# Performance work log

Measured on AMD Instinct MI355X. Metric: run time of the kernel, lower is better.

The kernel has to match this reference:

```python
import jax, jax.numpy as jnp
import numpy as np

B, C, H, W = 4, 64, 64, 64
CQK = C // 8


def setup_inputs() -> dict:
    key = jax.random.key(0)
    ks = jax.random.split(key, 4)
    x = jax.random.normal(ks[0], (B, C, H, W), dtype=jnp.float32)
    Wq = jax.random.normal(ks[1], (CQK, C), dtype=jnp.float32) * (1.0 / np.sqrt(C))
    bq = jnp.zeros((CQK,), dtype=jnp.float32)
    Wk = jax.random.normal(ks[2], (CQK, C), dtype=jnp.float32) * (1.0 / np.sqrt(C))
    bk = jnp.zeros((CQK,), dtype=jnp.float32)
    Wv = jax.random.normal(ks[3], (C, C), dtype=jnp.float32) * (1.0 / np.sqrt(C))
    bv = jnp.zeros((C,), dtype=jnp.float32)
    gamma = jnp.ones((1,), dtype=jnp.float32)
    return {"x": x, "Wq": Wq, "bq": bq, "Wk": Wk, "bk": bk,
            "Wv": Wv, "bv": bv, "gamma": gamma}


def reference(x, Wq, bq, Wk, bk, Wv, bv, gamma):
    b, c, h, w = x.shape
    n = h * w
    xf = x.reshape(b, c, n)                      # [B, C, N]
    # 1x1 convs == per-pixel linear over channels
    q = jnp.einsum('oc,bcn->bon', Wq, xf) + bq[:, None]   # [B, C/8, N]
    k = jnp.einsum('oc,bcn->bon', Wk, xf) + bk[:, None]   # [B, C/8, N]
    v = jnp.einsum('oc,bcn->bon', Wv, xf) + bv[:, None]   # [B, C, N]
    # attention_map[b,i,j] = <q[:, i], k[:, j]>; softmax over j
    attn = jax.nn.softmax(jnp.einsum('bci,bcj->bij', q, k), axis=-1)  # [B, N, N]
    # out[b,c,i] = sum_j v[b,c,j] * attn[b,i,j]  (bmm(V, attn^T))
    out = jnp.einsum('bcj,bij->bci', v, attn).reshape(b, c, h, w)
    return gamma * out + x
```

## Files before the change

kernel.cpp:

```cpp
#include <hip/hip_runtime.h>
#include <hip/hip_bf16.h>
#include <math.h>

#define NPIX 4096

typedef __attribute__((ext_vector_type(8))) short s8;
typedef __attribute__((ext_vector_type(16))) float f16v;

static __device__ __forceinline__ unsigned packbf2(float a, float b) {
    union { __hip_bfloat162 h; unsigned u; } x;
    x.h = __float22bfloat162_rn(make_float2(a, b));
    return x.u;
}
static __device__ __forceinline__ float fexp2(float x) {
#if __has_builtin(__builtin_amdgcn_exp2f)
    return __builtin_amdgcn_exp2f(x);
#else
    return exp2f(x);
#endif
}

static __device__ __forceinline__ void lane_swap(unsigned a, unsigned b, int lh,
                                                 unsigned &x, unsigned &y) {
#if __has_builtin(__builtin_amdgcn_permlane32_swap)
    auto r = __builtin_amdgcn_permlane32_swap((int)a, (int)b, false, false);
    x = (unsigned)r[0];
    y = (unsigned)r[1];
#else
    unsigned sa = __shfl_xor(a, 32), sb = __shfl_xor(b, 32);
    x = lh ? sb : a;
    y = lh ? b : sa;
#endif
}

__global__ __launch_bounds__(512) void prep_kernel(
    const float* __restrict__ x,
    const float* __restrict__ Wq, const float* __restrict__ bq,
    const float* __restrict__ Wk, const float* __restrict__ bk,
    __hip_bfloat16* __restrict__ qbf, __hip_bfloat16* __restrict__ kbf,
    __hip_bfloat16* __restrict__ xbf)
{
    __shared__ float Xp[64][65];
    __shared__ unsigned short Qs[64][8];
    int t = threadIdx.x;
    int p = t & 63;
    int g = t >> 6;
    int bid = blockIdx.x;
    int og = bid & 1;
    int n0 = ((bid >> 1) & 63) << 6;
    int b  = bid >> 7;

    const float* xb = x + ((size_t)b << 18);
    __hip_bfloat16* xbb = xbf + ((size_t)b << 18);
#pragma unroll
    for (int u = 0; u < 8; ++u) {
        int c = g + (u << 3);
        float v = xb[((size_t)c << 12) + n0 + p];
        Xp[c][p] = v;
        if ((og == 0) ? (u < 4) : (u >= 4))
            xbb[((size_t)c << 12) + n0 + p] = __float2bfloat16(v);
    }
    __syncthreads();

    const float* W  = og ? Wk : Wq;
    const float* bb = og ? bk : bq;
    const float* wr = W + g * 64;
    float acc = bb[g];
#pragma unroll
    for (int c = 0; c < 64; ++c) acc = fmaf(wr[c], Xp[c][p], acc);
    if (!og) acc *= 1.4426950408889634f;

    union { __hip_bfloat16 h; unsigned short u; } cv;
    cv.h = __float2bfloat16(acc);
    Qs[p][g] = cv.u;
    __syncthreads();

    if (t < 64) {
        __hip_bfloat16* dst = (og ? kbf : qbf) + ((size_t)(b * NPIX + n0 + t) << 3);
        *(s8*)dst = *(const s8*)&Qs[t][0];
    }
}

__global__ __launch_bounds__(512, 4) void flash_fused_kernel(
    const __hip_bfloat16* __restrict__ qbf, const __hip_bfloat16* __restrict__ kbf,
    const __hip_bfloat16* __restrict__ xbf,
    const float* __restrict__ Wv, const float* __restrict__ bv,
    const float* __restrict__ x, const float* __restrict__ gamma,
    float* __restrict__ out)
{
    __shared__ __align__(16) char pool[35200];
    unsigned short* Xs = (unsigned short*)pool;

    int t = threadIdx.x;
    int w    = t >> 6;
    int lane = t & 63;
    int l32  = lane & 31;
    int lh   = lane >> 5;

    int b  = blockIdx.x >> 7;
    int i0 = (blockIdx.x & 127) << 5;

    const s8 zero8 = {0, 0, 0, 0, 0, 0, 0, 0};

    s8 qf;
    {
        s8 qv = *(const s8*)(qbf + ((size_t)(b * NPIX + i0 + l32) << 3));
        qf = (lh == 0) ? qv : zero8;
    }

    f16v acc[2];
    f16v zero16;
#pragma unroll
    for (int r = 0; r < 16; ++r) { acc[0][r] = 0.f; acc[1][r] = 0.f; zero16[r] = 0.f; }
    float lsum = 0.f;

    const __hip_bfloat16* kb = kbf + ((size_t)(b * NPIX) << 3);
    const unsigned short* xg = (const unsigned short*)xbf + ((size_t)b << 18);

    int c = (w << 3) + (t & 7), seg = (t >> 3) & 7;
    const unsigned short* xsrc = xg + ((size_t)c << 12) + seg * 32;
    int xdst = c * 260 + seg * 32;

    uint2 pv[8];
    s8 kf;
    {
        const unsigned short* p = xsrc;
#pragma unroll
        for (int u = 0; u < 8; ++u) pv[u] = *(const uint2*)(p + u * 4);
        kf = *(const s8*)(kb + ((size_t)(w * 32 + l32) << 3));
    }

    for (int jt = 0; jt < 16; ++jt) {
        __syncthreads();

        {
            unsigned short* dstp = Xs + xdst;
#pragma unroll
            for (int u = 0; u < 8; ++u) *(uint2*)(dstp + u * 4) = pv[u];
        }

        f16v sC = __builtin_amdgcn_mfma_f32_32x32x16_bf16(kf, qf, zero16, 0, 0, 0);
        float e[16];
#pragma unroll
        for (int r = 0; r < 16; ++r) e[r] = fexp2(sC[r]);
#pragma unroll
        for (int r = 0; r < 16; ++r) lsum += e[r];
        unsigned P2[8];
#pragma unroll
        for (int s = 0; s < 8; ++s) P2[s] = packbf2(e[2 * s], e[2 * s + 1]);

        __syncthreads();

        {
            int jn = ((jt + 1) & 15) << 8;
            const unsigned short* p = xsrc + jn;
#pragma unroll
            for (int u = 0; u < 8; ++u) pv[u] = *(const uint2*)(p + u * 4);
            kf = *(const s8*)(kb + ((size_t)(jn + w * 32 + l32) << 3));
        }

        unsigned b00, b01, b02, b03, b10, b11, b12, b13;
        lane_swap(P2[0], P2[2], lh, b00, b02);
        lane_swap(P2[1], P2[3], lh, b01, b03);
        lane_swap(P2[4], P2[6], lh, b10, b12);
        lane_swap(P2[5], P2[7], lh, b11, b13);
        union { unsigned u[4]; s8 v; } bf0, bf1;
        bf0.u[0] = b00; bf0.u[1] = b01; bf0.u[2] = b02; bf0.u[3] = b03;
        bf1.u[0] = b10; bf1.u[1] = b11; bf1.u[2] = b12; bf1.u[3] = b13;

#pragma unroll
        for (int cm = 0; cm < 2; ++cm) {
            const unsigned short* xrow = Xs + (cm * 32 + l32) * 260 + w * 32 + lh * 8;
            union { uint2 u2[2]; s8 v; } xu0, xu1;
            xu0.u2[0] = *(const uint2*)(xrow);
            xu0.u2[1] = *(const uint2*)(xrow + 4);
            acc[cm] = __builtin_amdgcn_mfma_f32_32x32x16_bf16(xu0.v, bf0.v, acc[cm], 0, 0, 0);
            xu1.u2[0] = *(const uint2*)(xrow + 16);
            xu1.u2[1] = *(const uint2*)(xrow + 20);
            acc[cm] = __builtin_amdgcn_mfma_f32_32x32x16_bf16(xu1.v, bf1.v, acc[cm], 0, 0, 0);
        }
    }

    float* OshA = (float*)pool;
    float* OshB = (float*)(pool + 8704);
    float* Linv = (float*)(pool + 17408);
    float* bvs  = (float*)(pool + 17536);
    float* Wvs  = (float*)(pool + 17792);
    float* Lsh  = (float*)(pool + 34176);

    lsum += __shfl_xor(lsum, 32);
    if (lh == 0) Lsh[w * 32 + l32] = lsum;

    float* Og = (w >> 2) ? OshB : OshA;
    for (int s = 0; s < 4; ++s) {
        __syncthreads();
        if ((w & 3) == s) {
#pragma unroll
            for (int cm = 0; cm < 2; ++cm)
#pragma unroll
                for (int r = 0; r < 16; ++r) {
                    int cc = cm * 32 + (r & 3) + 8 * (r >> 2) + 4 * lh;
                    float* p = Og + l32 * 68 + cc;
                    if (s == 0) *p = acc[cm][r];
                    else        *p += acc[cm][r];
                }
        }
    }
    __syncthreads();

    if (t < 32) {
        float lt = 0.f;
#pragma unroll
        for (int ww = 0; ww < 8; ++ww) lt += Lsh[ww * 32 + t];
        Linv[t] = 1.0f / lt;
    }
    if (t < 64) bvs[t] = bv[t];
    {
        const float4* wsrc = (const float4*)Wv;
        float4* wdst = (float4*)Wvs;
        wdst[t] = wsrc[t];
        wdst[t + 512] = wsrc[t + 512];
    }
    __syncthreads();

    {
        int i  = t & 31;
        int cg = t >> 5;
        float inv = Linv[i];
        float res[4] = {0.f, 0.f, 0.f, 0.f};
#pragma unroll 4
        for (int cb = 0; cb < 16; ++cb) {
            float4 oa = *(const float4*)(OshA + i * 68 + cb * 4);
            float4 ob = *(const float4*)(OshB + i * 68 + cb * 4);
            float4 o = make_float4(oa.x + ob.x, oa.y + ob.y, oa.z + ob.z, oa.w + ob.w);
#pragma unroll
            for (int k = 0; k < 4; ++k) {
                const float4 wv4 = *(const float4*)(Wvs + (cg * 4 + k) * 64 + cb * 4);
                res[k] = fmaf(wv4.x, o.x, fmaf(wv4.y, o.y, fmaf(wv4.z, o.z, fmaf(wv4.w, o.w, res[k]))));
            }
        }
        float g = gamma[0];
        const float* xr = x + ((size_t)b << 18) + i0;
        float* outp = out + ((size_t)b << 18) + i0;
#pragma unroll
        for (int k = 0; k < 4; ++k) {
            int cch = cg * 4 + k;
            float attn = fmaf(res[k], inv, bvs[cch]);
            size_t off = ((size_t)cch << 12) + i;
            outp[off] = fmaf(g, attn, xr[off]);
        }
    }
}

extern "C" void kernel_launch(void* const* d_in, const int* in_sizes, int n_in,
                              void* d_out, int out_size, void* d_ws, size_t ws_size,
                              hipStream_t stream) {
    const float* x     = (const float*)d_in[0];
    const float* Wq    = (const float*)d_in[1];
    const float* bq    = (const float*)d_in[2];
    const float* Wk    = (const float*)d_in[3];
    const float* bk    = (const float*)d_in[4];
    const float* Wv    = (const float*)d_in[5];
    const float* bv    = (const float*)d_in[6];
    const float* gamma = (const float*)d_in[7];
    float* out = (float*)d_out;

    __hip_bfloat16* qbf = (__hip_bfloat16*)d_ws;
    __hip_bfloat16* kbf = qbf + (size_t)4 * NPIX * 8;
    __hip_bfloat16* xbf = kbf + (size_t)4 * NPIX * 8;

    prep_kernel<<<512, 512, 0, stream>>>(x, Wq, bq, Wk, bk, qbf, kbf, xbf);
    flash_fused_kernel<<<512, 512, 0, stream>>>(qbf, kbf, xbf, Wv, bv, x, gamma, out);
}
```

Measured before the change: 113.8 us.

## Double-buffer X tiles in LDS via direct global-to-LDS loads with XOR swizzle

Replaces the register-staged single LDS buffer for X tiles with two LDS buffers filled by global_load_lds, which copies straight from global memory into LDS. Padding is replaced by an XOR swizzle on the LDS layout, and each tile step now needs one barrier instead of two. Loads for tile jt+2 are issued while tile jt+1 is being consumed, which hides memory latency and saves VGPRs and LDS store instructions. The trade-off is that LDS use grows to 64 KB per block, which limits how many blocks can be resident on a CU. Correctness also depends on the barrier waiting for the asynchronous LDS loads to finish.

```diff
diff --git a/kernel.cpp b/kernel.cpp
--- a/kernel.cpp
+++ b/kernel.cpp
@@ -6,6 +6,9 @@
 
 typedef __attribute__((ext_vector_type(8))) short s8;
 typedef __attribute__((ext_vector_type(16))) float f16v;
+
+typedef __attribute__((address_space(1))) const void glob_cv;
+typedef __attribute__((address_space(3))) void lds_v;
 
 static __device__ __forceinline__ unsigned packbf2(float a, float b) {
     union { __hip_bfloat162 h; unsigned u; } x;
@@ -17,6 +20,15 @@
     return __builtin_amdgcn_exp2f(x);
 #else
     return exp2f(x);
+#endif
+}
+
+static __device__ __forceinline__ void gl_lds16(const unsigned short* g,
+                                                unsigned short* l, int lane) {
+#if __has_builtin(__builtin_amdgcn_global_load_lds)
+    __builtin_amdgcn_global_load_lds((glob_cv*)g, (lds_v*)l, 16, 0, 0);
+#else
+    *(uint4*)(l + lane * 8) = *(const uint4*)g;
 #endif
 }
 
@@ -88,8 +100,9 @@
     const float* __restrict__ x, const float* __restrict__ gamma,
     float* __restrict__ out)
 {
-    __shared__ __align__(16) char pool[35200];
-    unsigned short* Xs = (unsigned short*)pool;
+    __shared__ __align__(16) char pool[65536];
+    unsigned short* Xs0 = (unsigned short*)pool;
+    unsigned short* Xs1 = Xs0 + 16384;
 
     int t = threadIdx.x;
     int w    = t >> 6;
@@ -117,69 +130,72 @@
     const __hip_bfloat16* kb = kbf + ((size_t)(b * NPIX) << 3);
     const unsigned short* xg = (const unsigned short*)xbf + ((size_t)b << 18);
 
-    int c = (w << 3) + (t & 7), seg = (t >> 3) & 7;
-    const unsigned short* xsrc = xg + ((size_t)c << 12) + seg * 32;
-    int xdst = c * 260 + seg * 32;
-
-    uint2 pv[8];
-    s8 kf;
-    {
-        const unsigned short* p = xsrc;
-#pragma unroll
-        for (int u = 0; u < 8; ++u) pv[u] = *(const uint2*)(p + u * 4);
-        kf = *(const s8*)(kb + ((size_t)(w * 32 + l32) << 3));
-    }
-
-    for (int jt = 0; jt < 16; ++jt) {
-        __syncthreads();
-
-        {
-            unsigned short* dstp = Xs + xdst;
-#pragma unroll
-            for (int u = 0; u < 8; ++u) *(uint2*)(dstp + u * 4) = pv[u];
-        }
-
-        f16v sC = __builtin_amdgcn_mfma_f32_32x32x16_bf16(kf, qf, zero16, 0, 0, 0);
-        float e[16];
-#pragma unroll
-        for (int r = 0; r < 16; ++r) e[r] = fexp2(sC[r]);
-#pragma unroll
-        for (int r = 0; r < 16; ++r) lsum += e[r];
-        unsigned P2[8];
-#pragma unroll
-        for (int s = 0; s < 8; ++s) P2[s] = packbf2(e[2 * s], e[2 * s + 1]);
-
-        __syncthreads();
-
-        {
-            int jn = ((jt + 1) & 15) << 8;
-            const unsigned short* p = xsrc + jn;
-#pragma unroll
-            for (int u = 0; u < 8; ++u) pv[u] = *(const uint2*)(p + u * 4);
-            kf = *(const s8*)(kb + ((size_t)(jn + w * 32 + l32) << 3));
-        }
-
-        unsigned b00, b01, b02, b03, b10, b11, b12, b13;
-        lane_swap(P2[0], P2[2], lh, b00, b02);
-        lane_swap(P2[1], P2[3], lh, b01, b03);
-        lane_swap(P2[4], P2[6], lh, b10, b12);
-        lane_swap(P2[5], P2[7], lh, b11, b13);
-        union { unsigned u[4]; s8 v; } bf0, bf1;
-        bf0.u[0] = b00; bf0.u[1] = b01; bf0.u[2] = b02; bf0.u[3] = b03;
-        bf1.u[0] = b10; bf1.u[1] = b11; bf1.u[2] = b12; bf1.u[3] = b13;
-
-#pragma unroll
-        for (int cm = 0; cm < 2; ++cm) {
-            const unsigned short* xrow = Xs + (cm * 32 + l32) * 260 + w * 32 + lh * 8;
-            union { uint2 u2[2]; s8 v; } xu0, xu1;
-            xu0.u2[0] = *(const uint2*)(xrow);
-            xu0.u2[1] = *(const uint2*)(xrow + 4);
-            acc[cm] = __builtin_amdgcn_mfma_f32_32x32x16_bf16(xu0.v, bf0.v, acc[cm], 0, 0, 0);
-            xu1.u2[0] = *(const uint2*)(xrow + 16);
-            xu1.u2[1] = *(const uint2*)(xrow + 20);
-            acc[cm] = __builtin_amdgcn_mfma_f32_32x32x16_bf16(xu1.v, bf1.v, acc[cm], 0, 0, 0);
-        }
-    }
+    int rhalf = lane >> 5, gl = lane & 31;
+    int offv[4];
+#pragma unroll
+    for (int u = 0; u < 4; ++u) {
+        int r = (w << 3) + (u << 1) + rhalf;
+        offv[u] = (r << 12) + ((gl ^ (r & 31)) << 3);
+    }
+    int g1o = ((4 * w + lh) ^ l32) << 3;
+    int g2o = ((4 * w + lh + 2) ^ l32) << 3;
+    int woff = w * 32 + l32;
+
+#define STAGE(BUF, JT) do {                                                  \
+        unsigned short* lb_ = (BUF) + (w << 11);                             \
+        _Pragma("unroll")                                                    \
+        for (int u_ = 0; u_ < 4; ++u_)                                       \
+            gl_lds16(xg + offv[u_] + (JT) * 256, lb_ + (u_ << 9), lane);     \
+    } while (0)
+
+#define BODY(XSB, KF, JT) do {                                               \
+        f16v sC = __builtin_amdgcn_mfma_f32_32x32x16_bf16(KF, qf, zero16, 0, 0, 0); \
+        float e_[16];                                                        \
+        _Pragma("unroll")                                                    \
+        for (int r_ = 0; r_ < 16; ++r_) e_[r_] = fexp2(sC[r_]);              \
+        _Pragma("unroll")                                                    \
+        for (int r_ = 0; r_ < 16; ++r_) lsum += e_[r_];                      \
+        unsigned P2[8];                                                      \
+        _Pragma("unroll")                                                    \
+        for (int s_ = 0; s_ < 8; ++s_) P2[s_] = packbf2(e_[2*s_], e_[2*s_+1]); \
+        unsigned b00,b01,b02,b03,b10,b11,b12,b13;                            \
+        lane_swap(P2[0], P2[2], lh, b00, b02);                               \
+        lane_swap(P2[1], P2[3], lh, b01, b03);                               \
+        lane_swap(P2[4], P2[6], lh, b10, b12);                               \
+        lane_swap(P2[5], P2[7], lh, b11, b13);                               \
+        union { unsigned u[4]; s8 v; } bf0, bf1;                             \
+        bf0.u[0]=b00; bf0.u[1]=b01; bf0.u[2]=b02; bf0.u[3]=b03;              \
+        bf1.u[0]=b10; bf1.u[1]=b11; bf1.u[2]=b12; bf1.u[3]=b13;              \
+        _Pragma("unroll")                                                    \
+        for (int cm_ = 0; cm_ < 2; ++cm_) {                                  \
+            const unsigned short* xr_ = (XSB) + ((cm_ * 32 + l32) << 8);     \
+            union { uint2 u2[2]; s8 v; } xu0, xu1;                           \
+            xu0.u2[0] = *(const uint2*)(xr_ + g1o);                          \
+            xu0.u2[1] = *(const uint2*)(xr_ + g1o + 4);                      \
+            acc[cm_] = __builtin_amdgcn_mfma_f32_32x32x16_bf16(xu0.v, bf0.v, acc[cm_], 0, 0, 0); \
+            xu1.u2[0] = *(const uint2*)(xr_ + g2o);                          \
+            xu1.u2[1] = *(const uint2*)(xr_ + g2o + 4);                      \
+            acc[cm_] = __builtin_amdgcn_mfma_f32_32x32x16_bf16(xu1.v, bf1.v, acc[cm_], 0, 0, 0); \
+        }                                                                    \
+        __syncthreads();                     \
+        if ((JT) < 14) {                                                     \
+            STAGE(XSB, (JT) + 2);                                            \
+            KF = *(const s8*)(kb + ((size_t)(((JT) + 2) * 256 + woff) << 3)); \
+        }                                                                    \
+    } while (0)
+
+    STAGE(Xs0, 0);
+    STAGE(Xs1, 1);
+    s8 kfA = *(const s8*)(kb + ((size_t)woff << 3));
+    s8 kfB = *(const s8*)(kb + ((size_t)(256 + woff) << 3));
+    __syncthreads();
+
+    for (int jt = 0; jt < 16; jt += 2) {
+        BODY(Xs0, kfA, jt);
+        BODY(Xs1, kfB, jt + 1);
+    }
+#undef BODY
+#undef STAGE
 
     float* OshA = (float*)pool;
     float* OshB = (float*)(pool + 8704);
```

Result: faster. 101.2 us (-11.0%).
